# Kernel tuning notes

Measured on AMD Instinct MI355X. Metric: run time of the kernel, lower is better.

Reference implementation:

```python
import jax, jax.numpy as jnp
import numpy as np

B, S, D = 16, 2048, 1024   # batch, src_len, per-tensor feature dim (input_dim*growth_factor)
OUT = 1024                 # output_dim


def setup_inputs() -> dict:
    key = jax.random.key(0)
    k1, k2, k3, k4, k5, k6 = jax.random.split(key, 6)
    hidden = jax.random.normal(k1, (B, S, D), dtype=jnp.float32)
    encoder_outputs = jax.random.normal(k2, (B, S, D), dtype=jnp.float32)
    c_t = jax.random.normal(k3, (B, D), dtype=jnp.float32)
    # Linear(input_dim*3*growth_factor=3*D, OUT): PyTorch stores weight as [OUT, 3D]
    limit = 1.0 / np.sqrt(3 * D)
    W = jax.random.uniform(k4, (OUT, 3 * D), minval=-limit, maxval=limit, dtype=jnp.float32)
    b = jax.random.uniform(k5, (OUT,), minval=-limit, maxval=limit, dtype=jnp.float32)
    v = jax.random.uniform(k6, (OUT,), dtype=jnp.float32)  # torch.rand -> U[0,1)
    return {"hidden": hidden, "encoder_outputs": encoder_outputs, "c_t": c_t,
            "W": W, "b": b, "v": v}


def reference(hidden, encoder_outputs, c_t, W, b, v):
    # c_t broadcast over src_len; concat on feature dim -> [B, S, 3D]
    c_rep = jnp.broadcast_to(c_t[:, None, :], hidden.shape)
    cat = jnp.concatenate((hidden, c_rep, encoder_outputs), axis=2)
    # energy = relu(cat @ W^T + b): [B, S, OUT]
    energy = jax.nn.relu(jnp.einsum('bsf,of->bso', cat, W) + b)
    # attention = energy @ v: [B, S], then softmax over src_len
    attention = jnp.einsum('bso,o->bs', energy, v)
    return jax.nn.softmax(attention, axis=1)
```

## Files before the change

kernel.cpp:

```cpp
#include <hip/hip_runtime.h>
#include <hip/hip_bf16.h>


typedef __attribute__((ext_vector_type(8))) short short8;
typedef __attribute__((ext_vector_type(4))) float f32x4;
typedef __attribute__((ext_vector_type(8))) unsigned short ushort8v;
typedef __attribute__((ext_vector_type(4))) unsigned short ushort4v;

#define NB 16
#define NS 2048
#define ND 1024
#define NOUT 1024
#define NM (NB * NS)
#define KHE 2048

#define B8M 256
#define B8N 256
#define B8K 64
#define NT8 (KHE / B8K)

#define PREP_ACONV 16384
#define PREP_WCONV 2048
#define PREP_CBIAS 256
#define PREP_ZERO 32

__device__ __forceinline__ unsigned short bf16_rne(float x) {
    unsigned int u = __float_as_uint(x);
    unsigned int r = (u + 0x7fffu + ((u >> 16) & 1u)) >> 16;
    return (unsigned short)r;
}

__device__ __forceinline__ void gload_lds16(const unsigned short* g, unsigned short* l) {
    __builtin_amdgcn_global_load_lds(
        (const __attribute__((address_space(1))) void*)g,
        (__attribute__((address_space(3))) void*)l, 16, 0, 0);
}

__device__ __forceinline__ void bar_fence() {
    asm volatile("" ::: "memory");
    __builtin_amdgcn_s_barrier();
    asm volatile("" ::: "memory");
}

__global__ __launch_bounds__(256) void prep_k(const float* __restrict__ hidden,
                                              const float* __restrict__ enc,
                                              const float* __restrict__ c_t,
                                              const float* __restrict__ W,
                                              const float* __restrict__ bias,
                                              unsigned short* __restrict__ Abf,
                                              unsigned short* __restrict__ Wbf,
                                              float* __restrict__ cbias,
                                              float* __restrict__ logits) {
    const int bid = blockIdx.x;
    const int tid = threadIdx.x;
    if (bid < PREP_ACONV) {
        size_t c = (size_t)bid * 256 + tid;
        size_t m = c >> 7;
        int k = (int)(c & 127) * 16;
        const float* src = (k < ND) ? (hidden + m * ND + k) : (enc + m * ND + (k - ND));
        float4 f0 = ((const float4*)src)[0];
        float4 f1 = ((const float4*)src)[1];
        float4 f2 = ((const float4*)src)[2];
        float4 f3 = ((const float4*)src)[3];
        ushort8v h0, h1;
        h0[0] = bf16_rne(f0.x); h0[1] = bf16_rne(f0.y); h0[2] = bf16_rne(f0.z); h0[3] = bf16_rne(f0.w);
        h0[4] = bf16_rne(f1.x); h0[5] = bf16_rne(f1.y); h0[6] = bf16_rne(f1.z); h0[7] = bf16_rne(f1.w);
        h1[0] = bf16_rne(f2.x); h1[1] = bf16_rne(f2.y); h1[2] = bf16_rne(f2.z); h1[3] = bf16_rne(f2.w);
        h1[4] = bf16_rne(f3.x); h1[5] = bf16_rne(f3.y); h1[6] = bf16_rne(f3.z); h1[7] = bf16_rne(f3.w);
        *(ushort8v*)(Abf + m * KHE + k) = h0;
        *(ushort8v*)(Abf + m * KHE + k + 8) = h1;
    } else if (bid < PREP_ACONV + PREP_WCONV) {
        int idx = (bid - PREP_ACONV) * 256 + tid;
        int o = idx >> 9;
        int k = (idx & 511) * 4;
        int off = (k < ND) ? k : (k + ND);
        float4 f = *(const float4*)(W + (size_t)o * 3072 + off);
        ushort4v h;
        h.x = bf16_rne(f.x); h.y = bf16_rne(f.y); h.z = bf16_rne(f.z); h.w = bf16_rne(f.w);
        *(ushort4v*)(Wbf + (size_t)o * KHE + k) = h;
    } else if (bid < PREP_ACONV + PREP_WCONV + PREP_CBIAS) {
        int o = (bid - PREP_ACONV - PREP_WCONV) * 4 + (tid >> 6);
        int lane = tid & 63;
        const float* w = W + (size_t)o * 3072 + ND;
        float wr[16];
        #pragma unroll
        for (int j = 0; j < 16; ++j) wr[j] = w[lane + j * 64];
        float bo = bias[o];
        for (int b = 0; b < NB; ++b) {
            const float* cc = c_t + (size_t)b * ND;
            float s = 0.f;
            #pragma unroll
            for (int j = 0; j < 16; ++j) s = fmaf(cc[lane + j * 64], wr[j], s);
            #pragma unroll
            for (int m = 1; m < 64; m <<= 1) s += __shfl_xor(s, m);
            if (lane == 0) cbias[b * NOUT + o] = s + bo;
        }
    } else {
        int idx = (bid - PREP_ACONV - PREP_WCONV - PREP_CBIAS) * 256 + tid;
        ((float4*)logits)[idx] = make_float4(0.f, 0.f, 0.f, 0.f);
    }
}

__global__ __launch_bounds__(256) void wconv_k(const float* __restrict__ W,
                                               unsigned short* __restrict__ Wbf) {
    int idx = blockIdx.x * 256 + threadIdx.x;
    int o = idx >> 9;
    int k = (idx & 511) * 4;
    int off = (k < ND) ? k : (k + ND);
    float4 f = *(const float4*)(W + (size_t)o * 3072 + off);
    ushort4v h;
    h.x = bf16_rne(f.x); h.y = bf16_rne(f.y); h.z = bf16_rne(f.z); h.w = bf16_rne(f.w);
    *(ushort4v*)(Wbf + (size_t)o * KHE + k) = h;
}

__global__ __launch_bounds__(256) void cbias_k(const float* __restrict__ c_t,
                                               const float* __restrict__ W,
                                               const float* __restrict__ bias,
                                               float* __restrict__ cbias) {
    int o = blockIdx.x * 4 + (threadIdx.x >> 6);
    int lane = threadIdx.x & 63;
    const float* w = W + (size_t)o * 3072 + ND;
    float wr[16];
    #pragma unroll
    for (int j = 0; j < 16; ++j) wr[j] = w[lane + j * 64];
    float bo = bias[o];
    for (int b = 0; b < NB; ++b) {
        const float* c = c_t + (size_t)b * ND;
        float s = 0.f;
        #pragma unroll
        for (int j = 0; j < 16; ++j) s = fmaf(c[lane + j * 64], wr[j], s);
        #pragma unroll
        for (int m = 1; m < 64; m <<= 1) s += __shfl_xor(s, m);
        if (lane == 0) cbias[b * NOUT + o] = s + bo;
    }
}

__global__ __launch_bounds__(512, 2) void gemm8_k(const unsigned short* __restrict__ Abf,
                                                  const unsigned short* __restrict__ Wbf,
                                                  const float* __restrict__ cbias,
                                                  const float* __restrict__ v,
                                                  float* __restrict__ logits) {
    __shared__ unsigned short Ls[2][512][B8K] __attribute__((aligned(16)));
    __shared__ float rowsum[4][B8M];
    __shared__ float cb_s[B8N];
    __shared__ float v_s[B8N];

    const int tid = threadIdx.x;
    const int ntile = blockIdx.x & 3;
    const int mtile = blockIdx.x >> 2;
    const int m0 = mtile * B8M;
    const int o0 = ntile * B8N;
    const int batch = m0 >> 11;

    if (tid < B8N) {
        cb_s[tid] = cbias[batch * NOUT + o0 + tid];
        v_s[tid] = v[o0 + tid];
    }

    const int wid = tid >> 6;
    const int lane = tid & 63;
    const int wm = (wid & 1) * 128;
    const int wn = (wid >> 1) * 64;
    const int lr = lane >> 3;
    const int lc = (lane & 7) ^ lr;

    f32x4 acc[8][4] = {};
    short8 a[4][2], b[2][2];

    auto stageA = [&](int buf, int kt, int h) {
        #pragma unroll
        for (int t = 0; t < 2; ++t) {
            const int r0 = t * 128 + h * 64 + wid * 8;
            gload_lds16(Abf + (size_t)(m0 + r0 + lr) * KHE + kt + lc * 8, &Ls[buf][r0][0]);
        }
    };
    auto stageB = [&](int buf, int kt, int h) {
        #pragma unroll
        for (int t = 0; t < 2; ++t) {
            const int r0 = (wid >> 1) * 64 + h * 32 + (wid & 1) * 8 + t * 16;
            gload_lds16(Wbf + (size_t)(o0 + r0 + lr) * KHE + kt + lc * 8, &Ls[buf][256 + r0][0]);
        }
    };
    auto loadA = [&](int buf, int mh) {
        #pragma unroll
        for (int ks = 0; ks < 2; ++ks) {
            const int cb = ks * 4 + (lane >> 4);
            #pragma unroll
            for (int i = 0; i < 4; ++i) {
                const int row = wm + mh * 64 + i * 16 + (lane & 15);
                a[i][ks] = *(const short8*)&Ls[buf][row][(cb ^ (row & 7)) * 8];
            }
        }
    };
    auto loadB = [&](int buf, int nh) {
        #pragma unroll
        for (int ks = 0; ks < 2; ++ks) {
            const int cb = ks * 4 + (lane >> 4);
            #pragma unroll
            for (int j = 0; j < 2; ++j) {
                const int row = wn + nh * 32 + j * 16 + (lane & 15);
                b[j][ks] = *(const short8*)&Ls[buf][256 + row][(cb ^ (row & 7)) * 8];
            }
        }
    };
    auto mfma16 = [&](int mh, int nh) {
        __builtin_amdgcn_s_setprio(1);
        #pragma unroll
        for (int ks = 0; ks < 2; ++ks)
            #pragma unroll
            for (int i = 0; i < 4; ++i)
                #pragma unroll
                for (int j = 0; j < 2; ++j)
                    acc[mh * 4 + i][nh * 2 + j] = __builtin_amdgcn_mfma_f32_16x16x32_bf16(
                        a[i][ks], b[j][ks], acc[mh * 4 + i][nh * 2 + j], 0, 0, 0);
        __builtin_amdgcn_s_setprio(0);
    };

    stageA(0, 0, 0);
    stageB(0, 0, 0);
    stageB(0, 0, 1);
    stageA(0, 0, 1);
    asm volatile("s_waitcnt vmcnt(2)" ::: "memory");
    __builtin_amdgcn_s_barrier();
    asm volatile("" ::: "memory");

    #pragma unroll 2
    for (int t = 0; t < NT8; ++t) {
        const int cur = t & 1, nxt = cur ^ 1;
        const int kt1 = (t + 1) * B8K;
        const bool pf = (t + 1 < NT8);

        loadA(cur, 0);
        loadB(cur, 0);
        if (pf) stageA(nxt, kt1, 0);
        bar_fence();
        mfma16(0, 0);
        bar_fence();

        loadB(cur, 1);
        if (pf) stageB(nxt, kt1, 0);
        bar_fence();
        mfma16(0, 1);
        if (pf) asm volatile("s_waitcnt vmcnt(4)" ::: "memory");
        else    asm volatile("s_waitcnt vmcnt(0)" ::: "memory");
        bar_fence();

        loadA(cur, 1);
        if (pf) stageB(nxt, kt1, 1);
        bar_fence();
        mfma16(1, 1);
        bar_fence();

        loadB(cur, 0);
        if (pf) stageA(nxt, kt1, 1);
        bar_fence();
        mfma16(1, 0);
        asm volatile("s_waitcnt vmcnt(2)" ::: "memory");
        bar_fence();
    }

    __syncthreads();

    const int col = lane & 15;
    const int q = lane >> 4;
    float vv[4], cbv[4];
    #pragma unroll
    for (int j = 0; j < 4; ++j) {
        const int oc = wn + j * 16 + col;
        vv[j] = v_s[oc];
        cbv[j] = cb_s[oc];
    }
    #pragma unroll
    for (int i = 0; i < 8; ++i) {
        #pragma unroll
        for (int r = 0; r < 4; ++r) {
            float s = 0.f;
            #pragma unroll
            for (int j = 0; j < 4; ++j) {
                float e = acc[i][j][r] + cbv[j];
                e = fmaxf(e, 0.f);
                s = fmaf(e, vv[j], s);
            }
            s += __shfl_xor(s, 1);
            s += __shfl_xor(s, 2);
            s += __shfl_xor(s, 4);
            s += __shfl_xor(s, 8);
            if (col == 0) rowsum[wid >> 1][wm + i * 16 + q * 4 + r] = s;
        }
    }
    __syncthreads();
    if (tid < B8M)
        atomicAdd(&logits[m0 + tid],
                  rowsum[0][tid] + rowsum[1][tid] + rowsum[2][tid] + rowsum[3][tid]);
}

__global__ __launch_bounds__(256) void gemm_att_k(const float* __restrict__ hidden,
                                                  const float* __restrict__ enc,
                                                  const unsigned short* __restrict__ Wbf,
                                                  const float* __restrict__ Wf,
                                                  const float* __restrict__ cbias,
                                                  const float* __restrict__ v,
                                                  float* __restrict__ logits,
                                                  int use_wbf) {
    __shared__ unsigned short As[128 * 32] __attribute__((aligned(16)));
    __shared__ unsigned short Bs[128 * 32] __attribute__((aligned(16)));
    __shared__ float rowsum[2][128];
    __shared__ float cb_s[128];
    __shared__ float v_s[128];

    const int tid = threadIdx.x;
    const int ntile = blockIdx.x & 7;
    const int mtile = blockIdx.x >> 3;
    const int m0 = mtile * 128;
    const int o0 = ntile * 128;
    const int batch = m0 >> 11;

    if (tid < 128) {
        cb_s[tid] = cbias[batch * NOUT + o0 + tid];
        v_s[tid] = v[o0 + tid];
    }

    const int wid = tid >> 6;
    const int lane = tid & 63;
    const int wm = (wid & 1) * 64;
    const int wn = (wid >> 1) * 64;

    f32x4 acc[4][4] = {};

    for (int kt = 0; kt < KHE; kt += 32) {
        const float* Abase = (kt < ND) ? hidden : enc;
        const int aoff = (kt < ND) ? kt : (kt - ND);
        #pragma unroll
        for (int i = 0; i < 4; ++i) {
            int p = tid + i * 256;
            int row = p >> 3, kc = p & 7;
            float4 f = *(const float4*)(Abase + (size_t)(m0 + row) * ND + aoff + kc * 4);
            ushort4v h;
            h.x = bf16_rne(f.x); h.y = bf16_rne(f.y); h.z = bf16_rne(f.z); h.w = bf16_rne(f.w);
            *(ushort4v*)(As + row * 32 + kc * 4) = h;
        }
        if (use_wbf) {
            #pragma unroll
            for (int i = 0; i < 2; ++i) {
                int u = tid + i * 256;
                int ol = u >> 2, kc = u & 3;
                ushort8v w8 = *(const ushort8v*)(Wbf + (size_t)(o0 + ol) * KHE + kt + kc * 8);
                *(ushort8v*)(Bs + ol * 32 + kc * 8) = w8;
            }
        } else {
            const int woff = (kt < ND) ? kt : (kt + ND);
            #pragma unroll
            for (int i = 0; i < 4; ++i) {
                int p = tid + i * 256;
                int row = p >> 3, kc = p & 7;
                float4 f = *(const float4*)(Wf + (size_t)(o0 + row) * 3072 + woff + kc * 4);
                ushort4v h;
                h.x = bf16_rne(f.x); h.y = bf16_rne(f.y); h.z = bf16_rne(f.z); h.w = bf16_rne(f.w);
                *(ushort4v*)(Bs + row * 32 + kc * 4) = h;
            }
        }
        __syncthreads();

        short8 a_frag[4], b_frag[4];
        #pragma unroll
        for (int i = 0; i < 4; ++i)
            a_frag[i] = *(const short8*)(As + (wm + i * 16 + (lane & 15)) * 32 + (lane >> 4) * 8);
        #pragma unroll
        for (int j = 0; j < 4; ++j)
            b_frag[j] = *(const short8*)(Bs + (wn + j * 16 + (lane & 15)) * 32 + (lane >> 4) * 8);
        #pragma unroll
        for (int i = 0; i < 4; ++i)
            #pragma unroll
            for (int j = 0; j < 4; ++j)
                acc[i][j] = __builtin_amdgcn_mfma_f32_16x16x32_bf16(a_frag[i], b_frag[j],
                                                                    acc[i][j], 0, 0, 0);
        __syncthreads();
    }

    const int col = lane & 15;
    const int q = lane >> 4;
    float vv[4], cbv[4];
    #pragma unroll
    for (int j = 0; j < 4; ++j) {
        int oc = wn + j * 16 + col;
        vv[j] = v_s[oc];
        cbv[j] = cb_s[oc];
    }
    #pragma unroll
    for (int i = 0; i < 4; ++i) {
        #pragma unroll
        for (int r = 0; r < 4; ++r) {
            float s = 0.f;
            #pragma unroll
            for (int j = 0; j < 4; ++j) {
                float e = acc[i][j][r] + cbv[j];
                e = fmaxf(e, 0.f);
                s = fmaf(e, vv[j], s);
            }
            s += __shfl_xor(s, 1);
            s += __shfl_xor(s, 2);
            s += __shfl_xor(s, 4);
            s += __shfl_xor(s, 8);
            if (col == 0) rowsum[wid >> 1][wm + i * 16 + q * 4 + r] = s;
        }
    }
    __syncthreads();
    if (tid < 128) atomicAdd(&logits[m0 + tid], rowsum[0][tid] + rowsum[1][tid]);
}

__global__ __launch_bounds__(256) void softmax_k(const float* __restrict__ logits,
                                                 float* __restrict__ out) {
    const int b = blockIdx.x;
    const int tid = threadIdx.x;
    const int lane = tid & 63, wid = tid >> 6;
    __shared__ float redmax[4];
    __shared__ float redsum[4];
    const float* L = logits + (size_t)b * NS;
    float x[8];
    float mx = -3.4e38f;
    #pragma unroll
    for (int i = 0; i < 8; ++i) {
        x[i] = L[tid + i * 256];
        mx = fmaxf(mx, x[i]);
    }
    #pragma unroll
    for (int m = 1; m < 64; m <<= 1) mx = fmaxf(mx, __shfl_xor(mx, m));
    if (lane == 0) redmax[wid] = mx;
    __syncthreads();
    mx = fmaxf(fmaxf(redmax[0], redmax[1]), fmaxf(redmax[2], redmax[3]));
    float sum = 0.f;
    #pragma unroll
    for (int i = 0; i < 8; ++i) {
        x[i] = expf(x[i] - mx);
        sum += x[i];
    }
    #pragma unroll
    for (int m = 1; m < 64; m <<= 1) sum += __shfl_xor(sum, m);
    if (lane == 0) redsum[wid] = sum;
    __syncthreads();
    float inv = 1.0f / (redsum[0] + redsum[1] + redsum[2] + redsum[3]);
    #pragma unroll
    for (int i = 0; i < 8; ++i) out[(size_t)b * NS + tid + i * 256] = x[i] * inv;
}

extern "C" void kernel_launch(void* const* d_in, const int* in_sizes, int n_in,
                              void* d_out, int out_size, void* d_ws, size_t ws_size,
                              hipStream_t stream) {
    const float* hidden = (const float*)d_in[0];
    const float* enc    = (const float*)d_in[1];
    const float* c_t    = (const float*)d_in[2];
    const float* W      = (const float*)d_in[3];
    const float* bias   = (const float*)d_in[4];
    const float* v      = (const float*)d_in[5];
    float* out = (float*)d_out;

    char* ws = (char*)d_ws;
    float* logits = (float*)ws;
    float* cbias  = (float*)(ws + 131072);
    unsigned short* Wbf = (unsigned short*)(ws + 196608);
    unsigned short* Abf = (unsigned short*)(ws + 196608 + 4194304);
    const size_t need_wbf = 196608 + (size_t)NOUT * KHE * 2;
    const size_t need_abf = need_wbf + (size_t)NM * KHE * 2;

    if (ws_size >= need_abf) {
        prep_k<<<PREP_ACONV + PREP_WCONV + PREP_CBIAS + PREP_ZERO, 256, 0, stream>>>(
            hidden, enc, c_t, W, bias, Abf, Wbf, cbias, logits);
        gemm8_k<<<(NM / B8M) * (NOUT / B8N), 512, 0, stream>>>(Abf, Wbf, cbias, v, logits);
    } else if (ws_size >= need_wbf) {
        hipMemsetAsync(logits, 0, NM * sizeof(float), stream);
        cbias_k<<<NOUT / 4, 256, 0, stream>>>(c_t, W, bias, cbias);
        wconv_k<<<(NOUT * KHE / 4) / 256, 256, 0, stream>>>(W, Wbf);
        gemm_att_k<<<(NM / 128) * (NOUT / 128), 256, 0, stream>>>(hidden, enc, Wbf, W, cbias, v,
                                                                  logits, 1);
    } else {
        hipMemsetAsync(logits, 0, NM * sizeof(float), stream);
        cbias_k<<<NOUT / 4, 256, 0, stream>>>(c_t, W, bias, cbias);
        gemm_att_k<<<(NM / 128) * (NOUT / 128), 256, 0, stream>>>(hidden, enc, Wbf, W, cbias, v,
                                                                  logits, 0);
    }
    softmax_k<<<NB, 256, 0, stream>>>(logits, out);
}
```

Measured before the change: 443.4 us.

## Replace direct global-to-LDS loads with register-staged prefetch and single-barrier pipeline

Measured after the change: 426.6 us. -3.8%, faster.

```diff
diff --git a/kernel.cpp b/kernel.cpp
--- a/kernel.cpp
+++ b/kernel.cpp
@@ -28,18 +28,6 @@
     unsigned int u = __float_as_uint(x);
     unsigned int r = (u + 0x7fffu + ((u >> 16) & 1u)) >> 16;
     return (unsigned short)r;
-}
-
-__device__ __forceinline__ void gload_lds16(const unsigned short* g, unsigned short* l) {
-    __builtin_amdgcn_global_load_lds(
-        (const __attribute__((address_space(1))) void*)g,
-        (__attribute__((address_space(3))) void*)l, 16, 0, 0);
-}
-
-__device__ __forceinline__ void bar_fence() {
-    asm volatile("" ::: "memory");
-    __builtin_amdgcn_s_barrier();
-    asm volatile("" ::: "memory");
 }
 
 __global__ __launch_bounds__(256) void prep_k(const float* __restrict__ hidden,
@@ -165,98 +153,101 @@
     const int lc = (lane & 7) ^ lr;
 
     f32x4 acc[8][4] = {};
-    short8 a[4][2], b[2][2];
-
-    auto stageA = [&](int buf, int kt, int h) {
-        #pragma unroll
-        for (int t = 0; t < 2; ++t) {
-            const int r0 = t * 128 + h * 64 + wid * 8;
-            gload_lds16(Abf + (size_t)(m0 + r0 + lr) * KHE + kt + lc * 8, &Ls[buf][r0][0]);
+
+    auto gload = [&](int c, int kt) -> ushort8v {
+        if (c < 4) {
+            const int r0 = c * 64 + wid * 8;
+            return *(const ushort8v*)(Abf + (size_t)(m0 + r0 + lr) * KHE + kt + lc * 8);
+        } else {
+            const int r0 = (c - 4) * 64 + wid * 8;
+            return *(const ushort8v*)(Wbf + (size_t)(o0 + r0 + lr) * KHE + kt + lc * 8);
         }
     };
-    auto stageB = [&](int buf, int kt, int h) {
-        #pragma unroll
-        for (int t = 0; t < 2; ++t) {
-            const int r0 = (wid >> 1) * 64 + h * 32 + (wid & 1) * 8 + t * 16;
-            gload_lds16(Wbf + (size_t)(o0 + r0 + lr) * KHE + kt + lc * 8, &Ls[buf][256 + r0][0]);
-        }
+    auto swrite = [&](unsigned short* bufp, int c, ushort8v val) {
+        const int r0 = ((c < 4) ? c * 64 : 256 + (c - 4) * 64) + wid * 8;
+        *(ushort8v*)(bufp + (size_t)(r0 + lr) * B8K + (lane & 7) * 8) = val;
     };
-    auto loadA = [&](int buf, int mh) {
-        #pragma unroll
-        for (int ks = 0; ks < 2; ++ks) {
-            const int cb = ks * 4 + (lane >> 4);
-            #pragma unroll
-            for (int i = 0; i < 4; ++i) {
-                const int row = wm + mh * 64 + i * 16 + (lane & 15);
-                a[i][ks] = *(const short8*)&Ls[buf][row][(cb ^ (row & 7)) * 8];
-            }
+    auto loadAf = [&](const unsigned short* bufp, int mh, int ks, short8* d) {
+        const int cb = ks * 4 + (lane >> 4);
+        #pragma unroll
+        for (int i = 0; i < 4; ++i) {
+            const int row = wm + mh * 64 + i * 16 + (lane & 15);
+            d[i] = *(const short8*)(bufp + (size_t)row * B8K + (cb ^ (row & 7)) * 8);
         }
     };
-    auto loadB = [&](int buf, int nh) {
-        #pragma unroll
-        for (int ks = 0; ks < 2; ++ks) {
-            const int cb = ks * 4 + (lane >> 4);
-            #pragma unroll
-            for (int j = 0; j < 2; ++j) {
-                const int row = wn + nh * 32 + j * 16 + (lane & 15);
-                b[j][ks] = *(const short8*)&Ls[buf][256 + row][(cb ^ (row & 7)) * 8];
-            }
+    auto loadBf = [&](const unsigned short* bufp, int nh, int ks, short8* d) {
+        const int cb = ks * 4 + (lane >> 4);
+        #pragma unroll
+        for (int j = 0; j < 2; ++j) {
+            const int row = 256 + wn + nh * 32 + j * 16 + (lane & 15);
+            d[j] = *(const short8*)(bufp + (size_t)row * B8K + (cb ^ (row & 7)) * 8);
         }
     };
-    auto mfma16 = [&](int mh, int nh) {
+    auto mfma8 = [&](int mh, int nh, const short8* a4, const short8* b2) {
         __builtin_amdgcn_s_setprio(1);
         #pragma unroll
-        for (int ks = 0; ks < 2; ++ks)
-            #pragma unroll
-            for (int i = 0; i < 4; ++i)
-                #pragma unroll
-                for (int j = 0; j < 2; ++j)
-                    acc[mh * 4 + i][nh * 2 + j] = __builtin_amdgcn_mfma_f32_16x16x32_bf16(
-                        a[i][ks], b[j][ks], acc[mh * 4 + i][nh * 2 + j], 0, 0, 0);
+        for (int i = 0; i < 4; ++i)
+            #pragma unroll
+            for (int j = 0; j < 2; ++j)
+                acc[mh * 4 + i][nh * 2 + j] = __builtin_amdgcn_mfma_f32_16x16x32_bf16(
+                    a4[i], b2[j], acc[mh * 4 + i][nh * 2 + j], 0, 0, 0);
         __builtin_amdgcn_s_setprio(0);
     };
 
-    stageA(0, 0, 0);
-    stageB(0, 0, 0);
-    stageB(0, 0, 1);
-    stageA(0, 0, 1);
-    asm volatile("s_waitcnt vmcnt(2)" ::: "memory");
+    unsigned short* curp = &Ls[0][0][0];
+    unsigned short* nxtp = &Ls[1][0][0];
+
+    {
+        ushort8v g[8];
+        #pragma unroll
+        for (int c = 0; c < 8; ++c) g[c] = gload(c, 0);
+        #pragma unroll
+        for (int c = 0; c < 8; ++c) swrite(curp, c, g[c]);
+    }
+    asm volatile("s_waitcnt lgkmcnt(0)" ::: "memory");
     __builtin_amdgcn_s_barrier();
     asm volatile("" ::: "memory");
 
-    #pragma unroll 2
+    #pragma unroll 1
     for (int t = 0; t < NT8; ++t) {
-        const int cur = t & 1, nxt = cur ^ 1;
         const int kt1 = (t + 1) * B8K;
         const bool pf = (t + 1 < NT8);
-
-        loadA(cur, 0);
-        loadB(cur, 0);
-        if (pf) stageA(nxt, kt1, 0);
-        bar_fence();
-        mfma16(0, 0);
-        bar_fence();
-
-        loadB(cur, 1);
-        if (pf) stageB(nxt, kt1, 0);
-        bar_fence();
-        mfma16(0, 1);
-        if (pf) asm volatile("s_waitcnt vmcnt(4)" ::: "memory");
-        else    asm volatile("s_waitcnt vmcnt(0)" ::: "memory");
-        bar_fence();
-
-        loadA(cur, 1);
-        if (pf) stageB(nxt, kt1, 1);
-        bar_fence();
-        mfma16(1, 1);
-        bar_fence();
-
-        loadB(cur, 0);
-        if (pf) stageA(nxt, kt1, 1);
-        bar_fence();
-        mfma16(1, 0);
-        asm volatile("s_waitcnt vmcnt(2)" ::: "memory");
-        bar_fence();
+        short8 aA[4], aB[4], aC[4], aD[4], bA[2], bB[2], bC[2], bD[2];
+        ushort8v g0[4], g1[4];
+
+        if (pf) {
+            #pragma unroll
+            for (int c = 0; c < 4; ++c) g0[c] = gload(c, kt1);
+        }
+        loadAf(curp, 0, 0, aA);
+        loadBf(curp, 0, 0, bA);
+        loadBf(curp, 1, 0, bB);
+        mfma8(0, 0, aA, bA);
+        loadAf(curp, 1, 0, aB);
+        mfma8(0, 1, aA, bB);
+        loadAf(curp, 1, 1, aC);
+        loadBf(curp, 0, 1, bC);
+        mfma8(1, 1, aB, bB);
+        loadBf(curp, 1, 1, bD);
+        loadAf(curp, 0, 1, aD);
+        if (pf) {
+            #pragma unroll
+            for (int c = 0; c < 4; ++c) g1[c] = gload(c + 4, kt1);
+        }
+        mfma8(1, 0, aB, bA);
+        if (pf) { swrite(nxtp, 0, g0[0]); swrite(nxtp, 1, g0[1]); }
+        mfma8(1, 0, aC, bC);
+        if (pf) { swrite(nxtp, 2, g0[2]); swrite(nxtp, 3, g0[3]); }
+        mfma8(1, 1, aC, bD);
+        if (pf) { swrite(nxtp, 4, g1[0]); swrite(nxtp, 5, g1[1]); }
+        mfma8(0, 1, aD, bD);
+        if (pf) { swrite(nxtp, 6, g1[2]); swrite(nxtp, 7, g1[3]); }
+        mfma8(0, 0, aD, bC);
+
+        asm volatile("s_waitcnt lgkmcnt(0)" ::: "memory");
+        __builtin_amdgcn_s_barrier();
+        asm volatile("" ::: "memory");
+        unsigned short* tp = curp; curp = nxtp; nxtp = tp;
     }
 
     __syncthreads();
```

## Split LDS tiles into K-halves and restructure GEMM pipeline per k-subtile

Applied to the files above, without the earlier changes.

After: 452.7 us. 2.1% more time.

```diff
diff --git a/kernel.cpp b/kernel.cpp
--- a/kernel.cpp
+++ b/kernel.cpp
@@ -140,7 +140,7 @@
                                                   const float* __restrict__ cbias,
                                                   const float* __restrict__ v,
                                                   float* __restrict__ logits) {
-    __shared__ unsigned short Ls[2][512][B8K] __attribute__((aligned(16)));
+    __shared__ unsigned short Ls[2][2][512][32] __attribute__((aligned(16)));
     __shared__ float rowsum[4][B8M];
     __shared__ float cb_s[B8N];
     __shared__ float v_s[B8N];
@@ -161,102 +161,104 @@
     const int lane = tid & 63;
     const int wm = (wid & 1) * 128;
     const int wn = (wid >> 1) * 64;
-    const int lr = lane >> 3;
-    const int lc = (lane & 7) ^ lr;
+
+    const int srow = lane >> 2;
+    const int schunk = (lane & 3) ^ ((lane >> 3) & 3);
 
     f32x4 acc[8][4] = {};
-    short8 a[4][2], b[2][2];
-
-    auto stageA = [&](int buf, int kt, int h) {
+
+    auto stA = [&](int buf, int ktn, int ksh) {
         #pragma unroll
         for (int t = 0; t < 2; ++t) {
-            const int r0 = t * 128 + h * 64 + wid * 8;
-            gload_lds16(Abf + (size_t)(m0 + r0 + lr) * KHE + kt + lc * 8, &Ls[buf][r0][0]);
-        }
-    };
-    auto stageB = [&](int buf, int kt, int h) {
+            const int rb = wid * 32 + t * 16;
+            gload_lds16(Abf + (size_t)(m0 + rb + srow) * KHE + ktn + ksh * 32 + schunk * 8,
+                        &Ls[buf][ksh][rb][0]);
+        }
+    };
+    auto stB = [&](int buf, int ktn, int ksh) {
         #pragma unroll
         for (int t = 0; t < 2; ++t) {
-            const int r0 = (wid >> 1) * 64 + h * 32 + (wid & 1) * 8 + t * 16;
-            gload_lds16(Wbf + (size_t)(o0 + r0 + lr) * KHE + kt + lc * 8, &Ls[buf][256 + r0][0]);
-        }
-    };
-    auto loadA = [&](int buf, int mh) {
-        #pragma unroll
-        for (int ks = 0; ks < 2; ++ks) {
-            const int cb = ks * 4 + (lane >> 4);
-            #pragma unroll
-            for (int i = 0; i < 4; ++i) {
-                const int row = wm + mh * 64 + i * 16 + (lane & 15);
-                a[i][ks] = *(const short8*)&Ls[buf][row][(cb ^ (row & 7)) * 8];
-            }
-        }
-    };
-    auto loadB = [&](int buf, int nh) {
-        #pragma unroll
-        for (int ks = 0; ks < 2; ++ks) {
-            const int cb = ks * 4 + (lane >> 4);
-            #pragma unroll
-            for (int j = 0; j < 2; ++j) {
-                const int row = wn + nh * 32 + j * 16 + (lane & 15);
-                b[j][ks] = *(const short8*)&Ls[buf][256 + row][(cb ^ (row & 7)) * 8];
-            }
-        }
-    };
-    auto mfma16 = [&](int mh, int nh) {
+            const int rb = wid * 32 + t * 16;
+            gload_lds16(Wbf + (size_t)(o0 + rb + srow) * KHE + ktn + ksh * 32 + schunk * 8,
+                        &Ls[buf][ksh][256 + rb][0]);
+        }
+    };
+    auto rdA = [&](int buf, int ksh, int mh, short8* d) {
+        const int cb = lane >> 4;
+        #pragma unroll
+        for (int i = 0; i < 4; ++i) {
+            const int row = wm + mh * 64 + i * 16 + (lane & 15);
+            d[i] = *(const short8*)&Ls[buf][ksh][row][(cb ^ ((row >> 1) & 3)) * 8];
+        }
+    };
+    auto rdB = [&](int buf, int ksh, int nh, short8* d) {
+        const int cb = lane >> 4;
+        #pragma unroll
+        for (int j = 0; j < 2; ++j) {
+            const int row = wn + nh * 32 + j * 16 + (lane & 15);
+            d[j] = *(const short8*)&Ls[buf][ksh][256 + row][(cb ^ ((row >> 1) & 3)) * 8];
+        }
+    };
+    auto mm16 = [&](const short8* a4, const short8* b0, const short8* b1, int mh) {
         __builtin_amdgcn_s_setprio(1);
         #pragma unroll
-        for (int ks = 0; ks < 2; ++ks)
-            #pragma unroll
-            for (int i = 0; i < 4; ++i)
-                #pragma unroll
-                for (int j = 0; j < 2; ++j)
-                    acc[mh * 4 + i][nh * 2 + j] = __builtin_amdgcn_mfma_f32_16x16x32_bf16(
-                        a[i][ks], b[j][ks], acc[mh * 4 + i][nh * 2 + j], 0, 0, 0);
+        for (int i = 0; i < 4; ++i) {
+            #pragma unroll
+            for (int j = 0; j < 2; ++j)
+                acc[mh * 4 + i][j] = __builtin_amdgcn_mfma_f32_16x16x32_bf16(
+                    a4[i], b0[j], acc[mh * 4 + i][j], 0, 0, 0);
+            #pragma unroll
+            for (int j = 0; j < 2; ++j)
+                acc[mh * 4 + i][2 + j] = __builtin_amdgcn_mfma_f32_16x16x32_bf16(
+                    a4[i], b1[j], acc[mh * 4 + i][2 + j], 0, 0, 0);
+        }
         __builtin_amdgcn_s_setprio(0);
     };
 
-    stageA(0, 0, 0);
-    stageB(0, 0, 0);
-    stageB(0, 0, 1);
-    stageA(0, 0, 1);
-    asm volatile("s_waitcnt vmcnt(2)" ::: "memory");
+    stA(0, 0, 0);
+    stB(0, 0, 0);
+    stA(0, 0, 1);
+    stB(0, 0, 1);
+    asm volatile("s_waitcnt vmcnt(4)" ::: "memory");
     __builtin_amdgcn_s_barrier();
     asm volatile("" ::: "memory");
 
-    #pragma unroll 2
-    for (int t = 0; t < NT8; ++t) {
-        const int cur = t & 1, nxt = cur ^ 1;
-        const int kt1 = (t + 1) * B8K;
-        const bool pf = (t + 1 < NT8);
-
-        loadA(cur, 0);
-        loadB(cur, 0);
-        if (pf) stageA(nxt, kt1, 0);
-        bar_fence();
-        mfma16(0, 0);
-        bar_fence();
-
-        loadB(cur, 1);
-        if (pf) stageB(nxt, kt1, 0);
-        bar_fence();
-        mfma16(0, 1);
+    auto ktile = [&](int cbuf, int nbuf, int ktn, bool pf) {
+        short8 a0[4], a1[4], b0[2], b1[2];
+        rdA(cbuf, 0, 0, a0);
+        rdB(cbuf, 0, 0, b0);
+        rdB(cbuf, 0, 1, b1);
+        if (pf) stA(nbuf, ktn, 0);
+        bar_fence();
+        mm16(a0, b0, b1, 0);
+        bar_fence();
+        rdA(cbuf, 0, 1, a1);
+        if (pf) stB(nbuf, ktn, 0);
+        bar_fence();
+        mm16(a1, b0, b1, 1);
         if (pf) asm volatile("s_waitcnt vmcnt(4)" ::: "memory");
         else    asm volatile("s_waitcnt vmcnt(0)" ::: "memory");
         bar_fence();
-
-        loadA(cur, 1);
-        if (pf) stageB(nxt, kt1, 1);
-        bar_fence();
-        mfma16(1, 1);
-        bar_fence();
-
-        loadB(cur, 0);
-        if (pf) stageA(nxt, kt1, 1);
-        bar_fence();
-        mfma16(1, 0);
-        asm volatile("s_waitcnt vmcnt(2)" ::: "memory");
-        bar_fence();
+        rdA(cbuf, 1, 0, a0);
+        rdB(cbuf, 1, 0, b0);
+        rdB(cbuf, 1, 1, b1);
+        if (pf) stA(nbuf, ktn, 1);
+        bar_fence();
+        mm16(a0, b0, b1, 0);
+        bar_fence();
+        rdA(cbuf, 1, 1, a1);
+        if (pf) stB(nbuf, ktn, 1);
+        bar_fence();
+        mm16(a1, b0, b1, 1);
+        if (pf) asm volatile("s_waitcnt vmcnt(4)" ::: "memory");
+        bar_fence();
+    };
+
+    #pragma unroll 1
+    for (int it = 0; it < NT8 / 2; ++it) {
+        const bool last = (it == NT8 / 2 - 1);
+        ktile(0, 1, (2 * it + 1) * B8K, true);
+        ktile(1, 0, (2 * it + 2) * B8K, !last);
     }
 
     __syncthreads();
```
